# Optimization experiments

Hardware: AMD Instinct MI355X
Metric: run time of the kernel (lower is better)

## Reference

```python
import jax, jax.numpy as jnp
import numpy as np

B, S, D, H = 2, 2048, 1024, 16
DEPTH = D // H

def setup_inputs() -> dict:
    key = jax.random.key(0)
    ks = jax.random.split(key, 11)
    def glorot(k, shape):
        lim = np.sqrt(6.0 / (shape[0] + shape[1]))
        return jax.random.uniform(k, shape, jnp.float32, -lim, lim)
    return {
        'q': jax.random.normal(ks[0], (B, S, D), jnp.float32),
        'k': jax.random.normal(ks[1], (B, S, D), jnp.float32),
        'v': jax.random.normal(ks[2], (B, S, D), jnp.float32),
        'wq': glorot(ks[3], (D, D)), 'bq': jnp.zeros((D,), jnp.float32),
        'wk': glorot(ks[4], (D, D)), 'bk': jnp.zeros((D,), jnp.float32),
        'wv': glorot(ks[5], (D, D)), 'bv': jnp.zeros((D,), jnp.float32),
        'wo': glorot(ks[6], (D, D)), 'bo': jnp.zeros((D,), jnp.float32),
    }

def _split_heads(x):
    # [B,S,D] -> [B,H,S,depth]
    return x.reshape(B, S, H, DEPTH).transpose(0, 2, 1, 3)

def reference(q, k, v, wq, bq, wk, bk, wv, bv, wo, bo):
    qh = _split_heads(q @ wq + bq)
    kh = _split_heads(k @ wk + bk)
    vh = _split_heads(v @ wv + bv)
    scale = 1.0 / jnp.sqrt(jnp.float32(DEPTH))
    scores = jnp.einsum('bhqd,bhkd->bhqk', qh, kh) * scale
    attn = jax.nn.softmax(scores, axis=-1)
    out = jnp.einsum('bhqk,bhkd->bhqd', attn, vh)  # [B,H,S,depth]
    out = out.transpose(0, 2, 1, 3).reshape(B, S, D)
    return out @ wo + bo
```

## Files before the change

### kernel.cpp

```cpp
#include <hip/hip_runtime.h>
#include <hip/hip_bf16.h>
#include <stdint.h>

#define Bb 2
#define Ss 2048
#define Dd 1024
#define Hh 16

typedef __hip_bfloat16 bf16;
typedef __attribute__((ext_vector_type(8))) short bf16x8;
typedef __attribute__((ext_vector_type(4))) float f32x4;
typedef __attribute__((ext_vector_type(4))) unsigned uint4v;
typedef __attribute__((ext_vector_type(2))) unsigned uint2v;

__device__ __forceinline__ void gl_lds16(const void* g, void* l) {
  __builtin_amdgcn_global_load_lds((const __attribute__((address_space(1))) void*)g,
                                   (__attribute__((address_space(3))) void*)l, 16, 0, 0);
}

__device__ __forceinline__ unsigned pack2(float a, float b) {
  unsigned ua = __builtin_bit_cast(unsigned, a), ub = __builtin_bit_cast(unsigned, b);
  return ((ua + 0x8000u) >> 16) | ((ub + 0x8000u) & 0xffff0000u);
}

__device__ __forceinline__ bf16x8 lds_frag(const char* base, int row, int cl) {
  int phys = cl ^ (row & 7);
  return *(const bf16x8*)(base + row * 128 + phys * 16);
}

__global__ void convert_qk(const float* __restrict__ q, const float* __restrict__ k,
                           bf16* __restrict__ Qb, bf16* __restrict__ Kb) {
  int sel = blockIdx.x >> 11;
  const float* src = sel ? k : q;
  bf16* dst = sel ? Kb : Qb;
  size_t i = (size_t)(blockIdx.x & 2047) * 256 + threadIdx.x;
  f32x4 v0 = *(const f32x4*)(src + i * 8);
  f32x4 v1 = *(const f32x4*)(src + i * 8 + 4);
  uint4v o = {pack2(v0[0], v0[1]), pack2(v0[2], v0[3]),
              pack2(v1[0], v1[1]), pack2(v1[2], v1[3])};
  *(uint4v*)((char*)dst + i * 16) = o;
}

__global__ void transpose_w4(const float* w0, const float* w1, const float* w2, const float* w3,
                             bf16* t0, bf16* t1, bf16* t2, bf16* t3) {
  const float* W;
  bf16* T;
  switch (blockIdx.z) {
    case 0: W = w0; T = t0; break;
    case 1: W = w1; T = t1; break;
    case 2: W = w2; T = t2; break;
    default: W = w3; T = t3; break;
  }
  __shared__ bf16 tile[64][65];
  int tx = threadIdx.x, ty = threadIdx.y;
  int r0 = blockIdx.y * 64, c0 = blockIdx.x * 64;
#pragma unroll
  for (int j = 0; j < 16; j++) {
    int r = ty + j * 4;
    tile[r][tx] = __float2bfloat16(W[(size_t)(r0 + r) * 1024 + c0 + tx]);
  }
  __syncthreads();
#pragma unroll
  for (int j = 0; j < 16; j++) {
    int r = ty + j * 4;
    T[(size_t)(c0 + r) * 1024 + r0 + tx] = tile[tx][r];
  }
}

#define SCL 0.180336878f
__global__ __launch_bounds__(256, 3) void gemm_qkv(
    const bf16* __restrict__ Qb, const bf16* __restrict__ Kb, const float* __restrict__ v,
    const bf16* __restrict__ WTall,
    const float* __restrict__ bq, const float* __restrict__ bk, const float* __restrict__ bv,
    bf16* __restrict__ Qp, bf16* __restrict__ Kp, bf16* __restrict__ Vt) {
  __shared__ char As[128 * 128], Bs[128 * 128];
  const int K = 1024;
  int tid = threadIdx.x, lane = tid & 63, w = tid >> 6;
  int quad = lane >> 4, l16 = lane & 15;
  int xcd = blockIdx.x & 7, slot = blockIdx.x >> 3;
  int pair = xcd * 12 + (slot % 12);
  int nloc_blk = slot / 12;
  int mblk = pair / 3, sel = pair % 3;
  int m0 = mblk * 128;
  int nloc0 = nloc_blk * 128;
  int n0 = sel * 1024 + nloc0;
  const bf16* Ab = (sel == 0) ? Qb : Kb;
  const float* bias = (sel == 0) ? bq : (sel == 1) ? bk : bv;
  int wm = (w >> 1) * 64, wn = (w & 1) * 64;
  f32x4 acc[4][4] = {};
  for (int k0 = 0; k0 < K; k0 += 64) {
    __syncthreads();
    if (sel < 2) {
#pragma unroll
      for (int i = 0; i < 4; i++) {
        int c = i * 256 + tid;
        int row = c >> 3, cc = c & 7;
        int g = (cc ^ (row & 7)) * 16;
        gl_lds16((const char*)Ab + ((size_t)(m0 + row) * K + k0) * 2 + g, As + c * 16);
        gl_lds16((const char*)WTall + ((size_t)(n0 + row) * K + k0) * 2 + g, Bs + c * 16);
      }
    } else {
#pragma unroll
      for (int i = 0; i < 4; i++) {
        int c = i * 256 + tid;
        int row = c >> 3, cc = c & 7;
        int g = cc ^ (row & 7);
        const float* src = v + (size_t)(m0 + row) * K + k0 + g * 8;
        f32x4 v0 = *(const f32x4*)src;
        f32x4 v1 = *(const f32x4*)(src + 4);
        uint4v o = {pack2(v0[0], v0[1]), pack2(v0[2], v0[3]),
                    pack2(v1[0], v1[1]), pack2(v1[2], v1[3])};
        *(uint4v*)(As + c * 16) = o;
        gl_lds16((const char*)WTall + ((size_t)(n0 + row) * K + k0) * 2 + g * 16, Bs + c * 16);
      }
    }
    __syncthreads();
#pragma unroll
    for (int ks = 0; ks < 2; ks++) {
      bf16x8 a[4], b[4];
#pragma unroll
      for (int mt = 0; mt < 4; mt++) a[mt] = lds_frag(As, wm + mt * 16 + l16, ks * 4 + quad);
#pragma unroll
      for (int nt = 0; nt < 4; nt++) b[nt] = lds_frag(Bs, wn + nt * 16 + l16, ks * 4 + quad);
#pragma unroll
      for (int mt = 0; mt < 4; mt++)
#pragma unroll
        for (int nt = 0; nt < 4; nt++)
          acc[mt][nt] = __builtin_amdgcn_mfma_f32_16x16x32_bf16(a[mt], b[nt], acc[mt][nt], 0, 0, 0);
    }
  }
#pragma unroll
  for (int nt = 0; nt < 4; nt++) {
    int nloc = nloc0 + wn + nt * 16 + l16;
    float bvv = bias[nloc];
#pragma unroll
    for (int mt = 0; mt < 4; mt++) {
      int row = m0 + wm + mt * 16 + quad * 4;
      if (sel == 2) {
        int d = nloc & 63, h = nloc >> 6;
        int b_ = row >> 11, s = row & 2047;
        int bh = b_ * 16 + h;
        float f0 = acc[mt][nt][0] + bvv, f1 = acc[mt][nt][1] + bvv;
        float f2 = acc[mt][nt][2] + bvv, f3 = acc[mt][nt][3] + bvv;
        uint2v pv = {pack2(f0, f1), pack2(f2, f3)};
        *(uint2v*)((char*)Vt + ((size_t)(bh * 64 + d) * Ss + s) * 2) = pv;
      } else {
        bf16* C = (sel == 0) ? Qp : Kp;
        float scale = (sel == 0) ? SCL : 1.0f;
#pragma unroll
        for (int r = 0; r < 4; r++)
          C[(size_t)(row + r) * 1024 + nloc] = __float2bfloat16((acc[mt][nt][r] + bvv) * scale);
      }
    }
  }
}

__global__ __launch_bounds__(256, 2) void flash_attn(
    const bf16* __restrict__ Q, const bf16* __restrict__ Kp,
    const bf16* __restrict__ Vt, bf16* __restrict__ O) {
  __shared__ char lds[80 * 1024];
  char* Qs = lds;
  int tid = threadIdx.x, lane = tid & 63, w = tid >> 6;
  int quad = lane >> 4, l16 = lane & 15;
  int bx = blockIdx.x;
  int bh = bx & 31, b = bh >> 4, h = bh & 15;
  int q0 = (bx >> 5) * 128;
  int qw = (w & 1) * 64;
  int pair = w >> 1;
  char* Ps = lds + 48 * 1024 + pair * 16 * 1024;
  const char* Ksb = lds + 16 * 1024 + pair * 16 * 1024;
  const char* Vsb = Ksb + 8 * 1024;

#pragma unroll
  for (int i = 0; i < 4; i++) {
    int c = i * 256 + tid;
    int row = c >> 3, cc = c & 7;
    int gcol = (cc ^ (row & 7)) * 16;
    gl_lds16((const char*)Q + ((size_t)(b * Ss + q0 + row) * Dd + h * 64) * 2 + gcol, Qs + c * 16);
  }

  f32x4 o_acc[4][4] = {};
  f32x4 l_acc[4] = {};
  bf16x8 ones;
#pragma unroll
  for (int j = 0; j < 8; j++) ones[j] = (short)0x3F80;

  for (int kb0 = 0; kb0 < Ss / 64; kb0 += 2) {
    __syncthreads();
#pragma unroll
    for (int i = 0; i < 8; i++) {
      int c = i * 256 + tid;
      int bsel = i >> 1;
      int kbb = kb0 + (i >> 2);
      int c2 = c & 511;
      int row = c2 >> 3, cc = c2 & 7;
      int gcol = (cc ^ (row & 7)) * 16;
      char* dst = lds + 16 * 1024 + bsel * 8 * 1024 + c2 * 16;
      if ((bsel & 1) == 0)
        gl_lds16((const char*)Kp + ((size_t)(b * Ss + kbb * 64 + row) * Dd + h * 64) * 2 + gcol, dst);
      else
        gl_lds16((const char*)Vt + ((size_t)(bh * 64 + row) * Ss + kbb * 64) * 2 + gcol, dst);
    }
    __syncthreads();

    f32x4 s[4][4] = {};
#pragma unroll
    for (int ks = 0; ks < 2; ks++) {
      bf16x8 ak[4], bq[4];
#pragma unroll
      for (int kt = 0; kt < 4; kt++) ak[kt] = lds_frag(Ksb, kt * 16 + l16, ks * 4 + quad);
#pragma unroll
      for (int qt = 0; qt < 4; qt++) bq[qt] = lds_frag(Qs, qw + qt * 16 + l16, ks * 4 + quad);
#pragma unroll
      for (int kt = 0; kt < 4; kt++)
#pragma unroll
        for (int qt = 0; qt < 4; qt++)
          s[kt][qt] = __builtin_amdgcn_mfma_f32_16x16x32_bf16(ak[kt], bq[qt], s[kt][qt], 0, 0, 0);
    }

#pragma unroll
    for (int kt = 0; kt < 4; kt++)
#pragma unroll
      for (int qt = 0; qt < 4; qt++) {
        unsigned lo = pack2(exp2f(s[kt][qt][0]), exp2f(s[kt][qt][1]));
        unsigned hi = pack2(exp2f(s[kt][qt][2]), exp2f(s[kt][qt][3]));
        int row = qw + qt * 16 + l16;
        int cchunk = kt * 2 + (quad >> 1);
        int addr = row * 128 + ((cchunk ^ (row & 7)) * 16) + (quad & 1) * 8;
        uint2v pv = {lo, hi};
        *(uint2v*)(Ps + addr) = pv;
      }

    asm volatile("" ::: "memory");

#pragma unroll
    for (int ks = 0; ks < 2; ks++) {
      bf16x8 ap[4], bv[4];
#pragma unroll
      for (int mt = 0; mt < 4; mt++) ap[mt] = lds_frag(Ps, qw + mt * 16 + l16, ks * 4 + quad);
#pragma unroll
      for (int nt = 0; nt < 4; nt++) bv[nt] = lds_frag(Vsb, nt * 16 + l16, ks * 4 + quad);
#pragma unroll
      for (int mt = 0; mt < 4; mt++) {
#pragma unroll
        for (int nt = 0; nt < 4; nt++)
          o_acc[mt][nt] = __builtin_amdgcn_mfma_f32_16x16x32_bf16(ap[mt], bv[nt], o_acc[mt][nt], 0, 0, 0);
        l_acc[mt] = __builtin_amdgcn_mfma_f32_16x16x32_bf16(ap[mt], ones, l_acc[mt], 0, 0, 0);
      }
    }
  }

  __syncthreads();
  float* Obuf = (float*)(lds + 48 * 1024);
  float* Lbuf = (float*)(lds + 16 * 1024);
  if (pair == 1) {
#pragma unroll
    for (int mt = 0; mt < 4; mt++)
#pragma unroll
      for (int r = 0; r < 4; r++) {
        int qrow = qw + mt * 16 + quad * 4 + r;
#pragma unroll
        for (int nt = 0; nt < 4; nt++) Obuf[qrow * 64 + nt * 16 + l16] = o_acc[mt][nt][r];
        Lbuf[qrow] = l_acc[mt][r];
      }
  }
  __syncthreads();
  if (pair == 0) {
#pragma unroll
    for (int mt = 0; mt < 4; mt++)
#pragma unroll
      for (int r = 0; r < 4; r++) {
        int qrow = qw + mt * 16 + quad * 4 + r;
        float lt = l_acc[mt][r] + Lbuf[qrow];
        float inv = 1.0f / lt;
        int grow = b * Ss + q0 + qrow;
#pragma unroll
        for (int nt = 0; nt < 4; nt++) {
          float val = (o_acc[mt][nt][r] + Obuf[qrow * 64 + nt * 16 + l16]) * inv;
          O[(size_t)grow * Dd + h * 64 + nt * 16 + l16] = __float2bfloat16(val);
        }
      }
  }
}

__global__ __launch_bounds__(256, 2) void gemm_out(
    const bf16* __restrict__ AO, const bf16* __restrict__ WT,
    const float* __restrict__ bo, float* __restrict__ out) {
  __shared__ char As[128 * 128], Bs[64 * 128];
  const int K = 1024;
  int tid = threadIdx.x, lane = tid & 63, w = tid >> 6;
  int quad = lane >> 4, l16 = lane & 15;
  int xcd = blockIdx.x & 7, slot = blockIdx.x >> 3;
  int mblk = xcd * 4 + (slot & 3);
  int nblk = slot >> 2;
  int m0 = mblk * 128, n0 = nblk * 64;
  int wm = w * 32;
  f32x4 acc[2][4] = {};
  for (int k0 = 0; k0 < K; k0 += 64) {
    __syncthreads();
#pragma unroll
    for (int i = 0; i < 4; i++) {
      int c = i * 256 + tid;
      int row = c >> 3, cc = c & 7;
      int g = (cc ^ (row & 7)) * 16;
      gl_lds16((const char*)AO + ((size_t)(m0 + row) * K + k0) * 2 + g, As + c * 16);
    }
#pragma unroll
    for (int i = 0; i < 2; i++) {
      int c = i * 256 + tid;
      int row = c >> 3, cc = c & 7;
      int g = (cc ^ (row & 7)) * 16;
      gl_lds16((const char*)WT + ((size_t)(n0 + row) * K + k0) * 2 + g, Bs + c * 16);
    }
    __syncthreads();
#pragma unroll
    for (int ks = 0; ks < 2; ks++) {
      bf16x8 a[2], b[4];
#pragma unroll
      for (int mt = 0; mt < 2; mt++) a[mt] = lds_frag(As, wm + mt * 16 + l16, ks * 4 + quad);
#pragma unroll
      for (int nt = 0; nt < 4; nt++) b[nt] = lds_frag(Bs, nt * 16 + l16, ks * 4 + quad);
#pragma unroll
      for (int mt = 0; mt < 2; mt++)
#pragma unroll
        for (int nt = 0; nt < 4; nt++)
          acc[mt][nt] = __builtin_amdgcn_mfma_f32_16x16x32_bf16(a[mt], b[nt], acc[mt][nt], 0, 0, 0);
    }
  }
#pragma unroll
  for (int nt = 0; nt < 4; nt++) {
    int col = n0 + nt * 16 + l16;
    float bvv = bo[col];
#pragma unroll
    for (int mt = 0; mt < 2; mt++) {
      int row = m0 + wm + mt * 16 + quad * 4;
#pragma unroll
      for (int r = 0; r < 4; r++)
        out[(size_t)(row + r) * 1024 + col] = acc[mt][nt][r] + bvv;
    }
  }
}

extern "C" void kernel_launch(void* const* d_in, const int* in_sizes, int n_in,
                              void* d_out, int out_size, void* d_ws, size_t ws_size,
                              hipStream_t stream) {
  const float* q  = (const float*)d_in[0];
  const float* k  = (const float*)d_in[1];
  const float* v  = (const float*)d_in[2];
  const float* wq = (const float*)d_in[3];
  const float* bq = (const float*)d_in[4];
  const float* wk = (const float*)d_in[5];
  const float* bk = (const float*)d_in[6];
  const float* wv = (const float*)d_in[7];
  const float* bv = (const float*)d_in[8];
  const float* wo = (const float*)d_in[9];
  const float* bo = (const float*)d_in[10];
  float* out = (float*)d_out;

  char* ws = (char*)d_ws;
  const size_t MB = (size_t)1024 * 1024;
  bf16* wtall = (bf16*)(ws + 0 * MB);
  bf16* wtq = wtall;
  bf16* wtk = (bf16*)(ws + 2 * MB);
  bf16* wtv = (bf16*)(ws + 4 * MB);
  bf16* wto = (bf16*)(ws + 6 * MB);
  bf16* Qp  = (bf16*)(ws + 8 * MB);
  bf16* AO  = Qp;
  bf16* Kp  = (bf16*)(ws + 16 * MB);
  bf16* Vt  = (bf16*)(ws + 24 * MB);
  bf16* Qb  = (bf16*)((char*)d_out + 0 * MB);
  bf16* Kb  = (bf16*)((char*)d_out + 8 * MB);

  dim3 tb(64, 4);
  convert_qk<<<4096, 256, 0, stream>>>(q, k, Qb, Kb);
  transpose_w4<<<dim3(16, 16, 4), tb, 0, stream>>>(wq, wk, wv, wo, wtq, wtk, wtv, wto);
  gemm_qkv<<<768, 256, 0, stream>>>(Qb, Kb, v, wtall, bq, bk, bv, Qp, Kp, Vt);
  flash_attn<<<512, 256, 0, stream>>>(Qp, Kp, Vt, AO);
  gemm_out<<<512, 256, 0, stream>>>(AO, wto, bo, out);
}
```

Measured before the change: 253.4 us.

## Keep P in registers for PV MFMA, widen attention blocks, shrink out-GEMM tiles

Flash attention now runs 8 waves per block, each owning 32 query rows, and drops the P round-trip through LDS. Exponentiated scores are packed straight into 16x16x16 MFMA A-operands, with V fragments read per key tile. LDS use drops from 80KB to 48KB to allow more resident blocks. The output GEMM moves from 128x64 to 64x64 tiles with a 2x2 wave layout and twice as many blocks, trading per-block reuse for occupancy and parallelism.

```diff
diff --git a/kernel.cpp b/kernel.cpp
--- a/kernel.cpp
+++ b/kernel.cpp
@@ -9,6 +9,7 @@
 
 typedef __hip_bfloat16 bf16;
 typedef __attribute__((ext_vector_type(8))) short bf16x8;
+typedef __attribute__((ext_vector_type(4))) short short4v;
 typedef __attribute__((ext_vector_type(4))) float f32x4;
 typedef __attribute__((ext_vector_type(4))) unsigned uint4v;
 typedef __attribute__((ext_vector_type(2))) unsigned uint2v;
@@ -155,181 +156,163 @@
   }
 }
 
-__global__ __launch_bounds__(256, 2) void flash_attn(
+__global__ __launch_bounds__(512, 4) void flash_attn(
     const bf16* __restrict__ Q, const bf16* __restrict__ Kp,
     const bf16* __restrict__ Vt, bf16* __restrict__ O) {
-  __shared__ char lds[80 * 1024];
-  char* Qs = lds;
+  __shared__ char lds[48 * 1024];
   int tid = threadIdx.x, lane = tid & 63, w = tid >> 6;
   int quad = lane >> 4, l16 = lane & 15;
   int bx = blockIdx.x;
   int bh = bx & 31, b = bh >> 4, h = bh & 15;
   int q0 = (bx >> 5) * 128;
-  int qw = (w & 1) * 64;
-  int pair = w >> 1;
-  char* Ps = lds + 48 * 1024 + pair * 16 * 1024;
-  const char* Ksb = lds + 16 * 1024 + pair * 16 * 1024;
+  int qw = (w & 3) * 32;
+  int parity = w >> 2;
+  const char* Ksb = lds + 16 * 1024 + parity * 16 * 1024;
   const char* Vsb = Ksb + 8 * 1024;
 
 #pragma unroll
-  for (int i = 0; i < 4; i++) {
-    int c = i * 256 + tid;
+  for (int i = 0; i < 2; i++) {
+    int c = i * 512 + tid;
     int row = c >> 3, cc = c & 7;
     int gcol = (cc ^ (row & 7)) * 16;
-    gl_lds16((const char*)Q + ((size_t)(b * Ss + q0 + row) * Dd + h * 64) * 2 + gcol, Qs + c * 16);
-  }
-
-  f32x4 o_acc[4][4] = {};
-  f32x4 l_acc[4] = {};
-  bf16x8 ones;
-#pragma unroll
-  for (int j = 0; j < 8; j++) ones[j] = (short)0x3F80;
+    gl_lds16((const char*)Q + ((size_t)(b * Ss + q0 + row) * Dd + h * 64) * 2 + gcol, lds + c * 16);
+  }
+
+  f32x4 o_acc[2][4] = {};
+  f32x4 l_acc[2] = {};
+  const short4v ones4 = {(short)0x3F80, (short)0x3F80, (short)0x3F80, (short)0x3F80};
 
   for (int kb0 = 0; kb0 < Ss / 64; kb0 += 2) {
     __syncthreads();
-#pragma unroll
-    for (int i = 0; i < 8; i++) {
-      int c = i * 256 + tid;
-      int bsel = i >> 1;
-      int kbb = kb0 + (i >> 2);
-      int c2 = c & 511;
-      int row = c2 >> 3, cc = c2 & 7;
+    {
+      int row = tid >> 3, cc = tid & 7;
       int gcol = (cc ^ (row & 7)) * 16;
-      char* dst = lds + 16 * 1024 + bsel * 8 * 1024 + c2 * 16;
-      if ((bsel & 1) == 0)
-        gl_lds16((const char*)Kp + ((size_t)(b * Ss + kbb * 64 + row) * Dd + h * 64) * 2 + gcol, dst);
-      else
-        gl_lds16((const char*)Vt + ((size_t)(bh * 64 + row) * Ss + kbb * 64) * 2 + gcol, dst);
-    }
-    __syncthreads();
-
-    f32x4 s[4][4] = {};
+#pragma unroll
+      for (int i = 0; i < 4; i++) {
+        int kbb = kb0 + (i >> 1);
+        char* dst = lds + 16 * 1024 + i * 8 * 1024 + tid * 16;
+        if ((i & 1) == 0)
+          gl_lds16((const char*)Kp + ((size_t)(b * Ss + kbb * 64 + row) * Dd + h * 64) * 2 + gcol, dst);
+        else
+          gl_lds16((const char*)Vt + ((size_t)(bh * 64 + row) * Ss + kbb * 64) * 2 + gcol, dst);
+      }
+    }
+    __syncthreads();
+
+    f32x4 s[4][2] = {};
 #pragma unroll
     for (int ks = 0; ks < 2; ks++) {
-      bf16x8 ak[4], bq[4];
+      bf16x8 ak[4], bq[2];
 #pragma unroll
       for (int kt = 0; kt < 4; kt++) ak[kt] = lds_frag(Ksb, kt * 16 + l16, ks * 4 + quad);
 #pragma unroll
-      for (int qt = 0; qt < 4; qt++) bq[qt] = lds_frag(Qs, qw + qt * 16 + l16, ks * 4 + quad);
+      for (int qt = 0; qt < 2; qt++) bq[qt] = lds_frag(lds, qw + qt * 16 + l16, ks * 4 + quad);
 #pragma unroll
       for (int kt = 0; kt < 4; kt++)
 #pragma unroll
-        for (int qt = 0; qt < 4; qt++)
+        for (int qt = 0; qt < 2; qt++)
           s[kt][qt] = __builtin_amdgcn_mfma_f32_16x16x32_bf16(ak[kt], bq[qt], s[kt][qt], 0, 0, 0);
     }
 
 #pragma unroll
-    for (int kt = 0; kt < 4; kt++)
-#pragma unroll
-      for (int qt = 0; qt < 4; qt++) {
-        unsigned lo = pack2(exp2f(s[kt][qt][0]), exp2f(s[kt][qt][1]));
-        unsigned hi = pack2(exp2f(s[kt][qt][2]), exp2f(s[kt][qt][3]));
-        int row = qw + qt * 16 + l16;
-        int cchunk = kt * 2 + (quad >> 1);
-        int addr = row * 128 + ((cchunk ^ (row & 7)) * 16) + (quad & 1) * 8;
-        uint2v pv = {lo, hi};
-        *(uint2v*)(Ps + addr) = pv;
-      }
-
-    asm volatile("" ::: "memory");
-
-#pragma unroll
-    for (int ks = 0; ks < 2; ks++) {
-      bf16x8 ap[4], bv[4];
-#pragma unroll
-      for (int mt = 0; mt < 4; mt++) ap[mt] = lds_frag(Ps, qw + mt * 16 + l16, ks * 4 + quad);
-#pragma unroll
-      for (int nt = 0; nt < 4; nt++) bv[nt] = lds_frag(Vsb, nt * 16 + l16, ks * 4 + quad);
-#pragma unroll
-      for (int mt = 0; mt < 4; mt++) {
-#pragma unroll
-        for (int nt = 0; nt < 4; nt++)
-          o_acc[mt][nt] = __builtin_amdgcn_mfma_f32_16x16x32_bf16(ap[mt], bv[nt], o_acc[mt][nt], 0, 0, 0);
-        l_acc[mt] = __builtin_amdgcn_mfma_f32_16x16x32_bf16(ap[mt], ones, l_acc[mt], 0, 0, 0);
-      }
+    for (int kt = 0; kt < 4; kt++) {
+      short4v af[2];
+#pragma unroll
+      for (int qt = 0; qt < 2; qt++) {
+        union { short4v s4; uint2v u2; } u;
+        u.u2[0] = pack2(exp2f(s[kt][qt][0]), exp2f(s[kt][qt][1]));
+        u.u2[1] = pack2(exp2f(s[kt][qt][2]), exp2f(s[kt][qt][3]));
+        af[qt] = u.s4;
+      }
+#pragma unroll
+      for (int nt = 0; nt < 4; nt++) {
+        int row = nt * 16 + l16;
+        int chunk = kt * 2 + (quad >> 1);
+        int addr = row * 128 + ((chunk ^ (row & 7)) * 16) + (quad & 1) * 8;
+        short4v bfv = *(const short4v*)(Vsb + addr);
+#pragma unroll
+        for (int qt = 0; qt < 2; qt++)
+          o_acc[qt][nt] = __builtin_amdgcn_mfma_f32_16x16x16bf16_1k(af[qt], bfv, o_acc[qt][nt], 0, 0, 0);
+      }
+#pragma unroll
+      for (int qt = 0; qt < 2; qt++)
+        l_acc[qt] = __builtin_amdgcn_mfma_f32_16x16x16bf16_1k(af[qt], ones4, l_acc[qt], 0, 0, 0);
     }
   }
 
   __syncthreads();
-  float* Obuf = (float*)(lds + 48 * 1024);
-  float* Lbuf = (float*)(lds + 16 * 1024);
-  if (pair == 1) {
-#pragma unroll
-    for (int mt = 0; mt < 4; mt++)
+  float* Obuf = (float*)lds;
+  float* Lbuf = (float*)(lds + 32 * 1024);
+  if (parity == 1) {
+#pragma unroll
+    for (int qt = 0; qt < 2; qt++)
 #pragma unroll
       for (int r = 0; r < 4; r++) {
-        int qrow = qw + mt * 16 + quad * 4 + r;
-#pragma unroll
-        for (int nt = 0; nt < 4; nt++) Obuf[qrow * 64 + nt * 16 + l16] = o_acc[mt][nt][r];
-        Lbuf[qrow] = l_acc[mt][r];
+        int qrow = qw + qt * 16 + quad * 4 + r;
+#pragma unroll
+        for (int nt = 0; nt < 4; nt++) Obuf[qrow * 64 + nt * 16 + l16] = o_acc[qt][nt][r];
+        Lbuf[qrow] = l_acc[qt][r];
       }
   }
   __syncthreads();
-  if (pair == 0) {
-#pragma unroll
-    for (int mt = 0; mt < 4; mt++)
+  if (parity == 0) {
+#pragma unroll
+    for (int qt = 0; qt < 2; qt++)
 #pragma unroll
       for (int r = 0; r < 4; r++) {
-        int qrow = qw + mt * 16 + quad * 4 + r;
-        float lt = l_acc[mt][r] + Lbuf[qrow];
-        float inv = 1.0f / lt;
+        int qrow = qw + qt * 16 + quad * 4 + r;
+        float inv = 1.0f / (l_acc[qt][r] + Lbuf[qrow]);
         int grow = b * Ss + q0 + qrow;
 #pragma unroll
         for (int nt = 0; nt < 4; nt++) {
-          float val = (o_acc[mt][nt][r] + Obuf[qrow * 64 + nt * 16 + l16]) * inv;
+          float val = (o_acc[qt][nt][r] + Obuf[qrow * 64 + nt * 16 + l16]) * inv;
           O[(size_t)grow * Dd + h * 64 + nt * 16 + l16] = __float2bfloat16(val);
         }
       }
   }
 }
 
-__global__ __launch_bounds__(256, 2) void gemm_out(
+__global__ __launch_bounds__(256, 4) void gemm_out(
     const bf16* __restrict__ AO, const bf16* __restrict__ WT,
     const float* __restrict__ bo, float* __restrict__ out) {
-  __shared__ char As[128 * 128], Bs[64 * 128];
+  __shared__ char As[64 * 128], Bs[64 * 128];
   const int K = 1024;
   int tid = threadIdx.x, lane = tid & 63, w = tid >> 6;
   int quad = lane >> 4, l16 = lane & 15;
   int xcd = blockIdx.x & 7, slot = blockIdx.x >> 3;
-  int mblk = xcd * 4 + (slot & 3);
-  int nblk = slot >> 2;
-  int m0 = mblk * 128, n0 = nblk * 64;
-  int wm = w * 32;
-  f32x4 acc[2][4] = {};
+  int mblk = xcd * 8 + (slot & 7);
+  int nblk = slot >> 3;
+  int m0 = mblk * 64, n0 = nblk * 64;
+  int wm = (w & 1) * 32, wn = (w >> 1) * 32;
+  f32x4 acc[2][2] = {};
   for (int k0 = 0; k0 < K; k0 += 64) {
     __syncthreads();
 #pragma unroll
-    for (int i = 0; i < 4; i++) {
+    for (int i = 0; i < 2; i++) {
       int c = i * 256 + tid;
       int row = c >> 3, cc = c & 7;
       int g = (cc ^ (row & 7)) * 16;
       gl_lds16((const char*)AO + ((size_t)(m0 + row) * K + k0) * 2 + g, As + c * 16);
-    }
-#pragma unroll
-    for (int i = 0; i < 2; i++) {
-      int c = i * 256 + tid;
-      int row = c >> 3, cc = c & 7;
-      int g = (cc ^ (row & 7)) * 16;
       gl_lds16((const char*)WT + ((size_t)(n0 + row) * K + k0) * 2 + g, Bs + c * 16);
     }
     __syncthreads();
 #pragma unroll
     for (int ks = 0; ks < 2; ks++) {
-      bf16x8 a[2], b[4];
+      bf16x8 a[2], b[2];
 #pragma unroll
       for (int mt = 0; mt < 2; mt++) a[mt] = lds_frag(As, wm + mt * 16 + l16, ks * 4 + quad);
 #pragma unroll
-      for (int nt = 0; nt < 4; nt++) b[nt] = lds_frag(Bs, nt * 16 + l16, ks * 4 + quad);
+      for (int nt = 0; nt < 2; nt++) b[nt] = lds_frag(Bs, wn + nt * 16 + l16, ks * 4 + quad);
 #pragma unroll
       for (int mt = 0; mt < 2; mt++)
 #pragma unroll
-        for (int nt = 0; nt < 4; nt++)
+        for (int nt = 0; nt < 2; nt++)
           acc[mt][nt] = __builtin_amdgcn_mfma_f32_16x16x32_bf16(a[mt], b[nt], acc[mt][nt], 0, 0, 0);
     }
   }
 #pragma unroll
-  for (int nt = 0; nt < 4; nt++) {
-    int col = n0 + nt * 16 + l16;
+  for (int nt = 0; nt < 2; nt++) {
+    int col = n0 + wn + nt * 16 + l16;
     float bvv = bo[col];
 #pragma unroll
     for (int mt = 0; mt < 2; mt++) {
@@ -375,6 +358,6 @@
   convert_qk<<<4096, 256, 0, stream>>>(q, k, Qb, Kb);
   transpose_w4<<<dim3(16, 16, 4), tb, 0, stream>>>(wq, wk, wv, wo, wtq, wtk, wtv, wto);
   gemm_qkv<<<768, 256, 0, stream>>>(Qb, Kb, v, wtall, bq, bk, bv, Qp, Kp, Vt);
-  flash_attn<<<512, 256, 0, stream>>>(Qp, Kp, Vt, AO);
-  gemm_out<<<512, 256, 0, stream>>>(AO, wto, bo, out);
-}
+  flash_attn<<<512, 512, 0, stream>>>(Qp, Kp, Vt, AO);
+  gemm_out<<<1024, 256, 0, stream>>>(AO, wto, bo, out);
+}
```

Result: faster. 245.0 us (-3.3%).
